# Kernel optimization log

Measured on AMD Instinct MI355X. Metric: run time of the kernel, lower is better.

## Reference

```python
import jax, jax.numpy as jnp
import numpy as np

B, T, I, H = 32, 2048, 512, 512


def setup_inputs() -> dict:
    key = jax.random.key(0)
    ks = jax.random.split(key, 5)
    s_ih = 1.0 / np.sqrt(H)
    return {
        "x_t": jax.random.normal(ks[0], (B, T, I), dtype=jnp.float32),
        # PyTorch LSTM params, gate order [i, f, g, o]
        "W_ih": jax.random.uniform(ks[1], (4 * H, I), minval=-s_ih, maxval=s_ih, dtype=jnp.float32),
        "W_hh": jax.random.uniform(ks[2], (4 * H, H), minval=-s_ih, maxval=s_ih, dtype=jnp.float32),
        "b_ih": jax.random.uniform(ks[3], (4 * H,), minval=-s_ih, maxval=s_ih, dtype=jnp.float32),
        "b_hh": jax.random.uniform(ks[4], (4 * H,), minval=-s_ih, maxval=s_ih, dtype=jnp.float32),
    }


def _lstm_last_h(x_t, W_ih, W_hh, b_ih, b_hh):
    Bx = x_t.shape[0]
    Hh = W_hh.shape[1]
    # Precompute input projections for all timesteps in one big GEMM: [B,T,4H]
    x_proj = jnp.einsum("bti,gi->btg", x_t, W_ih) + (b_ih + b_hh)

    def step(carry, xp_t):
        h, c = carry
        z = xp_t + h @ W_hh.T  # [B, 4H]
        i, f, g, o = jnp.split(z, 4, axis=-1)
        i = jax.nn.sigmoid(i)
        f = jax.nn.sigmoid(f)
        g = jnp.tanh(g)
        o = jax.nn.sigmoid(o)
        c = f * c + i * g
        h = o * jnp.tanh(c)
        return (h, c), None

    h0 = jnp.zeros((Bx, Hh), dtype=x_t.dtype)
    c0 = jnp.zeros((Bx, Hh), dtype=x_t.dtype)
    (h_T, _), _ = jax.lax.scan(step, (h0, c0), jnp.swapaxes(x_proj, 0, 1))
    return h_T[None, :, :]  # [1, B, H] to match torch (num_layers*dirs, B, H)


def reference(x_t, W_ih, W_hh, b_ih, b_hh):
    return _lstm_last_h(x_t, W_ih, W_hh, b_ih, b_hh)
```

## Files before the change

kernel.cpp:

```cpp
#include <hip/hip_runtime.h>


#define T_FULL 2048
#define CHUNK  128
#define NCHUNK 16
#define NBLK   32
#define NGEMM  224

typedef float  f32x4 __attribute__((ext_vector_type(4)));
typedef short  s16x8 __attribute__((ext_vector_type(8)));
typedef unsigned int u32;

#define MFMA16(a,b,c) __builtin_amdgcn_mfma_f32_16x16x32_bf16((a),(b),(c),0,0,0)

__device__ inline unsigned short f2bf(float f){
  unsigned u = __builtin_bit_cast(unsigned, f);
  u += 0x7fffu + ((u>>16)&1u);
  return (unsigned short)(u>>16);
}
__device__ inline float bf2f(unsigned short s){
  unsigned u = ((unsigned)s)<<16;
  return __builtin_bit_cast(float, u);
}
__device__ inline float sigmoid_(float x){
  x = fminf(fmaxf(x,-30.f),30.f);
  return 1.f/(1.f + __expf(-x));
}
__device__ inline float tanh_(float x){
  x = fminf(fmaxf(x,-15.f),15.f);
  float e = __expf(2.f*x);
  return (e-1.f)/(e+1.f);
}

__device__ void gemm_tile(const float* __restrict__ x, const float* __restrict__ Wih,
                          const float* __restrict__ bih, const float* __restrict__ bhh,
                          unsigned short* __restrict__ xp, int t0, int nx, int ny,
                          char* smem)
{
  unsigned short* At = (unsigned short*)smem;
  unsigned short* Bt = (unsigned short*)(smem + 17408);
  const int tid = threadIdx.x, lane = tid&63, w = tid>>6;
  const int l15 = lane&15, l4 = lane>>4;
  const int n0 = nx*64, m0 = ny*64;
  const int mbase = (w&1)*32, nbase = (w>>1)*32;

  f32x4 acc[2][2];
  #pragma unroll
  for (int mi=0; mi<2; ++mi)
    #pragma unroll
    for (int ni=0; ni<2; ++ni)
      acc[mi][ni] = (f32x4){0.f,0.f,0.f,0.f};

  for (int kb=0; kb<4; ++kb){
    #pragma unroll
    for (int it=0; it<4; ++it){
      int grp = it*256 + tid;
      int row = grp>>4, c8 = (grp&15)*8;
      {
        int m = m0 + row;
        size_t t = (size_t)t0 + (m>>5), b = (size_t)(m&31);
        const float* src = x + ((b*2048 + t)<<9) + kb*128 + c8;
        f32x4 v0 = *(const f32x4*)src, v1 = *(const f32x4*)(src+4);
        unsigned short* d = &At[row*136 + c8];
        d[0]=f2bf(v0[0]); d[1]=f2bf(v0[1]); d[2]=f2bf(v0[2]); d[3]=f2bf(v0[3]);
        d[4]=f2bf(v1[0]); d[5]=f2bf(v1[1]); d[6]=f2bf(v1[2]); d[7]=f2bf(v1[3]);
      }
      {
        const float* src = Wih + (size_t)(n0+row)*512 + kb*128 + c8;
        f32x4 v0 = *(const f32x4*)src, v1 = *(const f32x4*)(src+4);
        unsigned short* d = &Bt[row*136 + c8];
        d[0]=f2bf(v0[0]); d[1]=f2bf(v0[1]); d[2]=f2bf(v0[2]); d[3]=f2bf(v0[3]);
        d[4]=f2bf(v1[0]); d[5]=f2bf(v1[1]); d[6]=f2bf(v1[2]); d[7]=f2bf(v1[3]);
      }
    }
    __syncthreads();
    #pragma unroll
    for (int ks=0; ks<4; ++ks){
      s16x8 af0 = *(const s16x8*)&At[(mbase+   l15)*136 + ks*32 + l4*8];
      s16x8 af1 = *(const s16x8*)&At[(mbase+16+l15)*136 + ks*32 + l4*8];
      s16x8 bf0 = *(const s16x8*)&Bt[(nbase+   l15)*136 + ks*32 + l4*8];
      s16x8 bf1 = *(const s16x8*)&Bt[(nbase+16+l15)*136 + ks*32 + l4*8];
      acc[0][0] = MFMA16(af0,bf0,acc[0][0]);
      acc[0][1] = MFMA16(af0,bf1,acc[0][1]);
      acc[1][0] = MFMA16(af1,bf0,acc[1][0]);
      acc[1][1] = MFMA16(af1,bf1,acc[1][1]);
    }
    __syncthreads();
  }
  #pragma unroll
  for (int ni=0; ni<2; ++ni){
    int col = n0 + nbase + ni*16 + l15;
    float bias = bih[col] + bhh[col];
    #pragma unroll
    for (int mi=0; mi<2; ++mi){
      #pragma unroll
      for (int r=0; r<4; ++r){
        int mrow = m0 + mbase + mi*16 + l4*4 + r;
        xp[(size_t)mrow*2048 + col] = f2bf(acc[mi][ni][r] + bias);
      }
    }
  }
}

__global__ __launch_bounds__(256) void lstm_p1(
    const float* __restrict__ x, const float* __restrict__ Wih,
    const float* __restrict__ bih, const float* __restrict__ bhh,
    unsigned short* __restrict__ xp, int t0)
{
  __shared__ __align__(16) char smem[34816];
  gemm_tile(x, Wih, bih, bhh, xp, t0, blockIdx.x, blockIdx.y, smem);
}

__global__ __launch_bounds__(256,1) void lstm_fused(
    const unsigned short* __restrict__ xp_cur,
    const float* __restrict__ x, const float* __restrict__ Wih,
    const float* __restrict__ bih, const float* __restrict__ bhh,
    unsigned short* __restrict__ xp_next, const float* __restrict__ Whh,
    unsigned short* __restrict__ Hbuf, float* __restrict__ cst,
    u32* __restrict__ flag, float* __restrict__ out, int t0, int do_gemm)
{
  __shared__ __align__(16) char smem[41472];
  const int bid = blockIdx.x;

  if (bid >= NBLK){
    if (do_gemm){
      const int t0n = t0 + CHUNK;
      for (int tile = bid - NBLK; tile < 32*(CHUNK*32/64); tile += NGEMM)
        gemm_tile(x, Wih, bih, bhh, xp_next, t0n, tile & 31, tile >> 5, smem);
    }
    return;
  }

  char* Hl = smem;
  float (*zl)[68] = (float(*)[68])(smem + 32768);
  const int k = bid;
  const int tid = threadIdx.x;
  const int lane = tid & 63, w = tid >> 6;
  const int l15 = lane & 15, l4 = lane >> 4;
  const int mt = w & 1, gp = w >> 1;

  s16x8 wf[2][16];
  #pragma unroll
  for (int nt=0; nt<2; ++nt){
    int lrow = gp*32 + nt*16 + l15;
    int grow = (lrow>>4)*512 + k*16 + (lrow&15);
    const float* wr = Whh + (size_t)grow*512;
    #pragma unroll
    for (int ks=0; ks<16; ++ks){
      const float* s = wr + ks*32 + l4*8;
      f32x4 v0 = *(const f32x4*)s, v1 = *(const f32x4*)(s+4);
      s16x8 tv;
      tv[0]=(short)f2bf(v0[0]); tv[1]=(short)f2bf(v0[1]);
      tv[2]=(short)f2bf(v0[2]); tv[3]=(short)f2bf(v0[3]);
      tv[4]=(short)f2bf(v1[0]); tv[5]=(short)f2bf(v1[1]);
      tv[6]=(short)f2bf(v1[2]); tv[7]=(short)f2bf(v1[3]);
      wf[nt][ks] = tv;
    }
  }

  const int s_ = tid >> 3, a_ = tid & 7;
  const int ucol = k*16 + 2*a_;
  float c0 = cst[s_*512 + ucol], c1 = cst[s_*512 + ucol + 1];

  for (int tt=0; tt<CHUNK; ++tt){
    const int t = t0 + tt;

    unsigned int xq[4];
    #pragma unroll
    for (int g=0; g<4; ++g)
      xq[g] = *(const unsigned int*)(xp_cur + (size_t)(tt*32 + s_)*2048 + g*512 + ucol);

    if (t > 0){
      if (w == 0){
        u32 va = (lane < NBLK)
          ? __hip_atomic_load(&flag[lane<<5], __ATOMIC_RELAXED, __HIP_MEMORY_SCOPE_AGENT)
          : 0xffffffffu;
        for (;;){
          u32 vb = (lane < NBLK)
            ? __hip_atomic_load(&flag[lane<<5], __ATOMIC_RELAXED, __HIP_MEMORY_SCOPE_AGENT)
            : 0xffffffffu;
          if (__all(va >= (u32)t)) break;
          va = (lane < NBLK)
            ? __hip_atomic_load(&flag[lane<<5], __ATOMIC_RELAXED, __HIP_MEMORY_SCOPE_AGENT)
            : 0xffffffffu;
          if (__all(vb >= (u32)t)) break;
        }
        __builtin_amdgcn_fence(__ATOMIC_ACQUIRE, "agent");
      }
      __syncthreads();
    }

    {
      const char* hsrc = (const char*)(Hbuf + ((t+1)&1)*(32*512));
      #pragma unroll
      for (int it=0; it<8; ++it){
        int off = (it*256 + tid)*16;
        f32x4 v = *(const f32x4*)(hsrc + off);
        *(f32x4*)&Hl[off ^ (((off>>10)&7)<<4)] = v;
      }
    }
    __syncthreads();

    f32x4 acc0 = (f32x4){0.f,0.f,0.f,0.f};
    f32x4 acc1 = (f32x4){0.f,0.f,0.f,0.f};
    {
      const int row = mt*16 + l15;
      const int swz = (row&7)<<4;
      const int rbase = row<<10;
      #pragma unroll
      for (int ks=0; ks<16; ++ks){
        int cb = ks*64 + l4*16;
        s16x8 af = *(const s16x8*)&Hl[rbase | (cb ^ swz)];
        acc0 = MFMA16(af, wf[0][ks], acc0);
        acc1 = MFMA16(af, wf[1][ks], acc1);
      }
    }
    #pragma unroll
    for (int r=0; r<4; ++r){
      zl[mt*16 + l4*4 + r][gp*32 +      l15] = acc0[r];
      zl[mt*16 + l4*4 + r][gp*32 + 16 + l15] = acc1[r];
    }
    __syncthreads();

    float zi0 = zl[s_][ 0 + 2*a_    ] + bf2f((unsigned short)(xq[0]&0xffffu));
    float zi1 = zl[s_][ 0 + 2*a_ + 1] + bf2f((unsigned short)(xq[0]>>16));
    float zf0 = zl[s_][16 + 2*a_    ] + bf2f((unsigned short)(xq[1]&0xffffu));
    float zf1 = zl[s_][16 + 2*a_ + 1] + bf2f((unsigned short)(xq[1]>>16));
    float zg0 = zl[s_][32 + 2*a_    ] + bf2f((unsigned short)(xq[2]&0xffffu));
    float zg1 = zl[s_][32 + 2*a_ + 1] + bf2f((unsigned short)(xq[2]>>16));
    float zo0 = zl[s_][48 + 2*a_    ] + bf2f((unsigned short)(xq[3]&0xffffu));
    float zo1 = zl[s_][48 + 2*a_ + 1] + bf2f((unsigned short)(xq[3]>>16));

    float i0 = sigmoid_(zi0), f0 = sigmoid_(zf0), g0 = tanh_(zg0), o0 = sigmoid_(zo0);
    float i1 = sigmoid_(zi1), f1 = sigmoid_(zf1), g1 = tanh_(zg1), o1 = sigmoid_(zo1);
    c0 = f0*c0 + i0*g0;
    c1 = f1*c1 + i1*g1;
    float h0 = o0 * tanh_(c0);
    float h1 = o1 * tanh_(c1);

    {
      unsigned short* hdst = Hbuf + (t&1)*(32*512);
      unsigned int hp = (unsigned int)f2bf(h0) | ((unsigned int)f2bf(h1)<<16);
      __hip_atomic_store((unsigned int*)((char*)hdst + s_*1024 + ucol*2), hp,
                         __ATOMIC_RELAXED, __HIP_MEMORY_SCOPE_AGENT);
    }
    if (t == T_FULL-1){
      out[s_*512 + ucol    ] = h0;
      out[s_*512 + ucol + 1] = h1;
    }

    asm volatile("s_waitcnt vmcnt(0)" ::: "memory");
    __syncthreads();
    if (tid == 0)
      __hip_atomic_store(&flag[k<<5], (unsigned)(t+1),
                         __ATOMIC_RELAXED, __HIP_MEMORY_SCOPE_AGENT);
  }

  cst[s_*512 + ucol    ] = c0;
  cst[s_*512 + ucol + 1] = c1;
}

extern "C" void kernel_launch(void* const* d_in, const int* in_sizes, int n_in,
                              void* d_out, int out_size, void* d_ws, size_t ws_size,
                              hipStream_t stream)
{
  const float* x   = (const float*)d_in[0];
  const float* Wih = (const float*)d_in[1];
  const float* Whh = (const float*)d_in[2];
  const float* bih = (const float*)d_in[3];
  const float* bhh = (const float*)d_in[4];
  float* out = (float*)d_out;

  char* ws = (char*)d_ws;
  const size_t XPB = (size_t)CHUNK*32*2048*2;
  unsigned short* xp0  = (unsigned short*)ws;
  unsigned short* xp1  = (unsigned short*)(ws + XPB);
  unsigned short* Hbuf = (unsigned short*)(ws + 2*XPB);
  float*          cst  = (float*)(ws + 2*XPB + 65536);
  u32*            flag = (u32*)(ws + 2*XPB + 65536 + 65536);

  (void)hipMemsetAsync(Hbuf, 0, 65536 + 65536 + 4096, stream);

  lstm_p1<<<dim3(32, CHUNK*32/64), 256, 0, stream>>>(x, Wih, bih, bhh, xp0, 0);

  for (int c=0; c<NCHUNK; ++c){
    unsigned short* xc = (c & 1) ? xp1 : xp0;
    unsigned short* xn = (c & 1) ? xp0 : xp1;
    lstm_fused<<<256, 256, 0, stream>>>(xc, x, Wih, bih, bhh, xn, Whh,
                                        Hbuf, cst, flag, out, c*CHUNK,
                                        (c < NCHUNK-1) ? 1 : 0);
  }
}
```

Measured before the change: 6.088 ms.

## Remap W_hh rows so gate outputs stay in registers, dropping LDS staging

Reorders which W_hh rows each wave loads so that the MFMA accumulators hold the i/f/g/o gates of the same hidden unit. The four gates are then combined with lane shuffles instead of being written to a shared-memory z tile and read back. This removes one __syncthreads and an LDS round trip per timestep on the serial recurrence path. In exchange, the x-projection loads become scattered 2-byte reads, and the h stores need an extra shuffle so that only half the lanes write packed pairs.

```diff
diff --git a/kernel.cpp b/kernel.cpp
--- a/kernel.cpp
+++ b/kernel.cpp
@@ -119,7 +119,7 @@
     unsigned short* __restrict__ Hbuf, float* __restrict__ cst,
     u32* __restrict__ flag, float* __restrict__ out, int t0, int do_gemm)
 {
-  __shared__ __align__(16) char smem[41472];
+  __shared__ __align__(16) char smem[34816];
   const int bid = blockIdx.x;
 
   if (bid >= NBLK){
@@ -132,43 +132,52 @@
   }
 
   char* Hl = smem;
-  float (*zl)[68] = (float(*)[68])(smem + 32768);
   const int k = bid;
   const int tid = threadIdx.x;
   const int lane = tid & 63, w = tid >> 6;
   const int l15 = lane & 15, l4 = lane >> 4;
   const int mt = w & 1, gp = w >> 1;
-
-  s16x8 wf[2][16];
-  #pragma unroll
-  for (int nt=0; nt<2; ++nt){
-    int lrow = gp*32 + nt*16 + l15;
-    int grow = (lrow>>4)*512 + k*16 + (lrow&15);
-    const float* wr = Whh + (size_t)grow*512;
+  const int u  = l15 & 7, gpair = l15 >> 3;
+  const int U  = k*16 + gp*8 + u;
+  const int g0 = gpair, g1 = 2 + gpair;
+  const int bq = mt*16 + l4*4 + 2*gpair;
+
+  s16x8 wf0[16], wf1[16];
+  {
+    const float* w0 = Whh + (size_t)(g0*512 + U)*512 + l4*8;
+    const float* w1 = Whh + (size_t)(g1*512 + U)*512 + l4*8;
     #pragma unroll
     for (int ks=0; ks<16; ++ks){
-      const float* s = wr + ks*32 + l4*8;
-      f32x4 v0 = *(const f32x4*)s, v1 = *(const f32x4*)(s+4);
-      s16x8 tv;
-      tv[0]=(short)f2bf(v0[0]); tv[1]=(short)f2bf(v0[1]);
-      tv[2]=(short)f2bf(v0[2]); tv[3]=(short)f2bf(v0[3]);
-      tv[4]=(short)f2bf(v1[0]); tv[5]=(short)f2bf(v1[1]);
-      tv[6]=(short)f2bf(v1[2]); tv[7]=(short)f2bf(v1[3]);
-      wf[nt][ks] = tv;
-    }
-  }
-
-  const int s_ = tid >> 3, a_ = tid & 7;
-  const int ucol = k*16 + 2*a_;
-  float c0 = cst[s_*512 + ucol], c1 = cst[s_*512 + ucol + 1];
+      f32x4 a0 = *(const f32x4*)(w0 + ks*32), b0 = *(const f32x4*)(w0 + ks*32 + 4);
+      f32x4 a1 = *(const f32x4*)(w1 + ks*32), b1 = *(const f32x4*)(w1 + ks*32 + 4);
+      s16x8 t0v, t1v;
+      t0v[0]=(short)f2bf(a0[0]); t0v[1]=(short)f2bf(a0[1]);
+      t0v[2]=(short)f2bf(a0[2]); t0v[3]=(short)f2bf(a0[3]);
+      t0v[4]=(short)f2bf(b0[0]); t0v[5]=(short)f2bf(b0[1]);
+      t0v[6]=(short)f2bf(b0[2]); t0v[7]=(short)f2bf(b0[3]);
+      t1v[0]=(short)f2bf(a1[0]); t1v[1]=(short)f2bf(a1[1]);
+      t1v[2]=(short)f2bf(a1[2]); t1v[3]=(short)f2bf(a1[3]);
+      t1v[4]=(short)f2bf(b1[0]); t1v[5]=(short)f2bf(b1[1]);
+      t1v[6]=(short)f2bf(b1[2]); t1v[7]=(short)f2bf(b1[3]);
+      wf0[ks] = t0v; wf1[ks] = t1v;
+    }
+  }
+
+  float c0 = cst[(size_t)(bq  )*512 + U];
+  float c1 = cst[(size_t)(bq+1)*512 + U];
 
   for (int tt=0; tt<CHUNK; ++tt){
     const int t = t0 + tt;
 
-    unsigned int xq[4];
-    #pragma unroll
-    for (int g=0; g<4; ++g)
-      xq[g] = *(const unsigned int*)(xp_cur + (size_t)(tt*32 + s_)*2048 + g*512 + ucol);
+    float xg0[4], xg1[4];
+    {
+      const unsigned short* xr = xp_cur + (size_t)(tt*32 + mt*16 + l4*4)*2048;
+      #pragma unroll
+      for (int r=0; r<4; ++r){
+        xg0[r] = bf2f(xr[(size_t)r*2048 + g0*512 + U]);
+        xg1[r] = bf2f(xr[(size_t)r*2048 + g1*512 + U]);
+      }
+    }
 
     if (t > 0){
       if (w == 0){
@@ -211,53 +220,68 @@
       for (int ks=0; ks<16; ++ks){
         int cb = ks*64 + l4*16;
         s16x8 af = *(const s16x8*)&Hl[rbase | (cb ^ swz)];
-        acc0 = MFMA16(af, wf[0][ks], acc0);
-        acc1 = MFMA16(af, wf[1][ks], acc1);
-      }
-    }
+        acc0 = MFMA16(af, wf0[ks], acc0);
+        acc1 = MFMA16(af, wf1[ks], acc1);
+      }
+    }
+
+    float za0[4], za1[4], pa0[4], pa1[4];
     #pragma unroll
     for (int r=0; r<4; ++r){
-      zl[mt*16 + l4*4 + r][gp*32 +      l15] = acc0[r];
-      zl[mt*16 + l4*4 + r][gp*32 + 16 + l15] = acc1[r];
-    }
-    __syncthreads();
-
-    float zi0 = zl[s_][ 0 + 2*a_    ] + bf2f((unsigned short)(xq[0]&0xffffu));
-    float zi1 = zl[s_][ 0 + 2*a_ + 1] + bf2f((unsigned short)(xq[0]>>16));
-    float zf0 = zl[s_][16 + 2*a_    ] + bf2f((unsigned short)(xq[1]&0xffffu));
-    float zf1 = zl[s_][16 + 2*a_ + 1] + bf2f((unsigned short)(xq[1]>>16));
-    float zg0 = zl[s_][32 + 2*a_    ] + bf2f((unsigned short)(xq[2]&0xffffu));
-    float zg1 = zl[s_][32 + 2*a_ + 1] + bf2f((unsigned short)(xq[2]>>16));
-    float zo0 = zl[s_][48 + 2*a_    ] + bf2f((unsigned short)(xq[3]&0xffffu));
-    float zo1 = zl[s_][48 + 2*a_ + 1] + bf2f((unsigned short)(xq[3]>>16));
-
-    float i0 = sigmoid_(zi0), f0 = sigmoid_(zf0), g0 = tanh_(zg0), o0 = sigmoid_(zo0);
-    float i1 = sigmoid_(zi1), f1 = sigmoid_(zf1), g1 = tanh_(zg1), o1 = sigmoid_(zo1);
-    c0 = f0*c0 + i0*g0;
-    c1 = f1*c1 + i1*g1;
-    float h0 = o0 * tanh_(c0);
-    float h1 = o1 * tanh_(c1);
-
-    {
-      unsigned short* hdst = Hbuf + (t&1)*(32*512);
-      unsigned int hp = (unsigned int)f2bf(h0) | ((unsigned int)f2bf(h1)<<16);
-      __hip_atomic_store((unsigned int*)((char*)hdst + s_*1024 + ucol*2), hp,
-                         __ATOMIC_RELAXED, __HIP_MEMORY_SCOPE_AGENT);
+      za0[r] = acc0[r] + xg0[r];
+      za1[r] = acc1[r] + xg1[r];
+    }
+    #pragma unroll
+    for (int r=0; r<4; ++r){
+      pa0[r] = __shfl_xor(za0[r], 8);
+      pa1[r] = __shfl_xor(za1[r], 8);
+    }
+
+    float h0, h1;
+    {
+      float zi = gpair ? pa0[2] : za0[0];
+      float zf = gpair ? za0[2] : pa0[0];
+      float zg = gpair ? pa1[2] : za1[0];
+      float zo = gpair ? za1[2] : pa1[0];
+      float ii = sigmoid_(zi), ff = sigmoid_(zf), gg = tanh_(zg), oo = sigmoid_(zo);
+      c0 = ff*c0 + ii*gg;
+      h0 = oo * tanh_(c0);
+      zi = gpair ? pa0[3] : za0[1];
+      zf = gpair ? za0[3] : pa0[1];
+      zg = gpair ? pa1[3] : za1[1];
+      zo = gpair ? za1[3] : pa1[1];
+      ii = sigmoid_(zi); ff = sigmoid_(zf); gg = tanh_(zg); oo = sigmoid_(zo);
+      c1 = ff*c1 + ii*gg;
+      h1 = oo * tanh_(c1);
+    }
+
+    {
+      unsigned short* Hd = Hbuf + (t&1)*(32*512);
+      float h0p = __shfl_xor(h0, 1);
+      float h1p = __shfl_xor(h1, 1);
+      if ((u & 1) == 0){
+        u32 wd0 = (u32)f2bf(h0) | ((u32)f2bf(h0p) << 16);
+        u32 wd1 = (u32)f2bf(h1) | ((u32)f2bf(h1p) << 16);
+        __hip_atomic_store((u32*)(Hd + (size_t)(bq  )*512 + U), wd0,
+                           __ATOMIC_RELAXED, __HIP_MEMORY_SCOPE_AGENT);
+        __hip_atomic_store((u32*)(Hd + (size_t)(bq+1)*512 + U), wd1,
+                           __ATOMIC_RELAXED, __HIP_MEMORY_SCOPE_AGENT);
+      }
     }
     if (t == T_FULL-1){
-      out[s_*512 + ucol    ] = h0;
-      out[s_*512 + ucol + 1] = h1;
+      out[(size_t)(bq  )*512 + U] = h0;
+      out[(size_t)(bq+1)*512 + U] = h1;
     }
 
     asm volatile("s_waitcnt vmcnt(0)" ::: "memory");
     __syncthreads();
     if (tid == 0)
-      __hip_atomic_store(&flag[k<<5], (unsigned)(t+1),
+      __hip_atomic_store(&flag[k<<5], (u32)(t+1),
                          __ATOMIC_RELAXED, __HIP_MEMORY_SCOPE_AGENT);
   }
 
-  cst[s_*512 + ucol    ] = c0;
-  cst[s_*512 + ucol + 1] = c1;
+  cst[(size_t)(bq  )*512 + U] = c0;
+  cst[(size_t)(bq+1)*512 + U] = c1;
 }
 
 extern "C" void kernel_launch(void* const* d_in, const int* in_sizes, int n_in,
```

Result: no change. 6.194 ms (+1.7%).
